# Performance work log

Hardware: AMD Instinct MI355X
Metric: run time of the kernel (lower is better)

Reference implementation:

```python
import jax, jax.numpy as jnp
import numpy as np

B, S, D, H, F = 8, 1024, 1024, 16, 4096
DH = D // H
EPS = 1e-8
NEG_INF = -1e30


def setup_inputs() -> dict:
    key = jax.random.key(0)
    ks = jax.random.split(key, 12)
    x = jax.random.normal(ks[0], (B, S, D), jnp.float32)
    # variable valid lengths in [S//2, S]; True = keep (valid token)
    lengths = jax.random.randint(ks[1], (B,), S // 2, S + 1)
    src_key_padding_mask = jnp.arange(S)[None, :] < lengths[:, None]
    rel_pos_bias = 0.02 * jax.random.normal(ks[2], (1, H, S, S), jnp.float32)
    w = lambda k, sh, std: std * jax.random.normal(k, sh, jnp.float32)
    std = D ** -0.5
    return {
        'x': x,
        'src_key_padding_mask': src_key_padding_mask,
        'rel_pos_bias': rel_pos_bias,
        'Wq': w(ks[3], (D, D), std),
        'Wk': w(ks[4], (D, D), std),
        'Wv': w(ks[5], (D, D), std),
        'Wo': w(ks[6], (D, D), std),
        'g1': jnp.ones((D,), jnp.float32),
        'g2': jnp.ones((D,), jnp.float32),
        'W1': w(ks[7], (D, F), std),
        'b1': jnp.zeros((F,), jnp.float32),
        'W2': w(ks[8], (F, F and D), F ** -0.5),
        'b2': jnp.zeros((D,), jnp.float32),
    }


def rmsnorm(x, g):
    # x / sqrt(mean(x^2) + eps) * g   (no mean subtraction)
    ms = jnp.mean(x * x, axis=-1, keepdims=True)
    return x * jax.lax.rsqrt(ms + EPS) * g


def attention(h, kpm, rel_pos_bias, Wq, Wk, Wv, Wo):
    b, s, d = h.shape
    q = (h @ Wq).reshape(b, s, H, DH)
    k = (h @ Wk).reshape(b, s, H, DH)
    v = (h @ Wv).reshape(b, s, H, DH)
    scores = jnp.einsum('bqhd,bkhd->bhqk', q, k) / np.sqrt(DH)
    scores = scores + rel_pos_bias
    scores = jnp.where(kpm[:, None, None, :], scores, NEG_INF)
    attn = jax.nn.softmax(scores, axis=-1)
    out = jnp.einsum('bhqk,bkhd->bqhd', attn, v).reshape(b, s, d)
    return out @ Wo


def reference(x, src_key_padding_mask, rel_pos_bias,
              Wq, Wk, Wv, Wo, g1, g2, W1, b1, W2, b2):
    h = rmsnorm(x, g1)
    x = x + attention(h, src_key_padding_mask, rel_pos_bias, Wq, Wk, Wv, Wo)
    h = rmsnorm(x, g2)
    ff = jax.nn.relu(h @ W1 + b1) @ W2 + b2
    return x + ff
```

## Files before the change

### kernel.cpp

```cpp
#include <hip/hip_runtime.h>
#include <stdint.h>

typedef __bf16 bf16;
typedef __bf16 bf16x4 __attribute__((ext_vector_type(4)));
typedef __bf16 bf16x8 __attribute__((ext_vector_type(8)));
typedef float f32x4 __attribute__((ext_vector_type(4)));

constexpr int Bz = 8, S = 1024, D = 1024, NH = 16, DH = 64, F = 4096;

__device__ __forceinline__ bool is_f32(const uint16_t* dt) { return dt[0] == 0; }

__device__ __forceinline__ void ld4(const void* p, size_t idx, bool f32, float o[4]) {
  if (f32) {
    float4 v = *(const float4*)((const float*)p + idx);
    o[0] = v.x; o[1] = v.y; o[2] = v.z; o[3] = v.w;
  } else {
    bf16x4 v = *(const bf16x4*)((const bf16*)p + idx);
    o[0] = v[0]; o[1] = v[1]; o[2] = v[2]; o[3] = v[3];
  }
}

__device__ __forceinline__ float ld1(const void* p, size_t idx, bool f32) {
  return f32 ? ((const float*)p)[idx] : (float)((const bf16*)p)[idx];
}

__device__ __forceinline__ void gload_lds16(const bf16* g, bf16* l) {
  __builtin_amdgcn_global_load_lds(
      (const __attribute__((address_space(1))) void*)g,
      (__attribute__((address_space(3))) void*)l, 16, 0, 0);
}

__global__ void lengths_kernel(const unsigned char* __restrict__ mask,
                               int* __restrict__ lengths) {
  int b = blockIdx.x;
  int esz = (mask[1] == 1) ? 1 : ((mask[1] != 0) ? 2 : 4);
  int cnt = 0;
  for (int s = threadIdx.x; s < S; s += blockDim.x) {
    const unsigned char* p = mask + ((size_t)b * S + s) * esz;
    unsigned v = 0;
    for (int j = 0; j < esz; j++) v |= p[j];
    cnt += (v != 0) ? 1 : 0;
  }
#pragma unroll
  for (int m = 32; m >= 1; m >>= 1) cnt += __shfl_xor(cnt, m);
  __shared__ int sred[4];
  if ((threadIdx.x & 63) == 0) sred[threadIdx.x >> 6] = cnt;
  __syncthreads();
  if (threadIdx.x == 0) lengths[b] = sred[0] + sred[1] + sred[2] + sred[3];
}

__global__ void transpose_any(const void* __restrict__ src, bf16* __restrict__ dst,
                              int R, int C, const uint16_t* __restrict__ dt) {
  bool f32 = is_f32(dt);
  __shared__ bf16 tile[64][65];
  int c0 = blockIdx.x * 64, r0 = blockIdx.y * 64;
  int tx = threadIdx.x, ty = threadIdx.y;
#pragma unroll
  for (int i = 0; i < 4; i++) {
    int r = ty * 4 + i;
    float v[4];
    ld4(src, (size_t)(r0 + r) * C + c0 + tx * 4, f32, v);
#pragma unroll
    for (int j = 0; j < 4; j++) tile[r][tx * 4 + j] = (bf16)v[j];
  }
  __syncthreads();
#pragma unroll
  for (int i = 0; i < 4; i++) {
    int rr = ty * 4 + i;
    bf16x4 ov;
#pragma unroll
    for (int j = 0; j < 4; j++) ov[j] = tile[tx * 4 + j][rr];
    *(bf16x4*)(dst + (size_t)(c0 + rr) * R + r0 + tx * 4) = ov;
  }
}

__global__ void bias_cvt(const void* __restrict__ src, bf16* __restrict__ dst,
                         const uint16_t* __restrict__ dt) {
  bool f32 = is_f32(dt);
  size_t i = ((size_t)blockIdx.x * 256 + threadIdx.x) * 4;
  float v[4];
  ld4(src, i, f32, v);
  bf16x4 o;
#pragma unroll
  for (int j = 0; j < 4; j++) o[j] = (bf16)v[j];
  *(bf16x4*)(dst + i) = o;
}

template <bool ADD>
__global__ void rmsnorm_kernel(const void* __restrict__ xv, const bf16* __restrict__ add,
                               const void* __restrict__ gv, bf16* __restrict__ y,
                               const uint16_t* __restrict__ dt) {
  bool f32 = is_f32(dt);
  int row = blockIdx.x, t = threadIdx.x;
  float xf[4];
  ld4(xv, (size_t)row * D + t * 4, f32, xf);
  if (ADD) {
    bf16x4 a = *(const bf16x4*)(add + (size_t)row * D + t * 4);
#pragma unroll
    for (int j = 0; j < 4; j++) xf[j] += (float)a[j];
  }
  float ss = xf[0] * xf[0] + xf[1] * xf[1] + xf[2] * xf[2] + xf[3] * xf[3];
#pragma unroll
  for (int m = 32; m >= 1; m >>= 1) ss += __shfl_xor(ss, m);
  __shared__ float sred[4];
  if ((t & 63) == 0) sred[t >> 6] = ss;
  __syncthreads();
  float tot = sred[0] + sred[1] + sred[2] + sred[3];
  float scale = rsqrtf(tot * (1.0f / D) + 1e-8f);
  float gf[4];
  ld4(gv, (size_t)t * 4, f32, gf);
  bf16x4 ov;
#pragma unroll
  for (int j = 0; j < 4; j++) ov[j] = (bf16)(xf[j] * scale * gf[j]);
  *(bf16x4*)(y + (size_t)row * D + t * 4) = ov;
}

template <bool BIAS, bool RELU, bool RES1, bool RES2, bool OUTEXT, bool VT>
__global__ void gemm_nt(const bf16* __restrict__ A, const bf16* __restrict__ Bt,
                        void* __restrict__ Cv, const void* __restrict__ biasv,
                        const void* __restrict__ res1, const bf16* __restrict__ res2,
                        int M, int N, int K, const uint16_t* __restrict__ dt) {
  bool f32 = is_f32(dt);
  __shared__ bf16 As[2 * 4096];
  __shared__ bf16 Bs[2 * 4096];
  const int tid = threadIdx.x, lane = tid & 63, w = tid >> 6;
  const int wm = w >> 1, wn = w & 1;
  const int lid = blockIdx.x;
  const int bm = ((lid & 7) << 3) + ((lid >> 3) & 7);
  const int bn = lid >> 6;
  const int quad = lane >> 4, c = lane & 15;

  f32x4 acc[4][4];
#pragma unroll
  for (int i = 0; i < 4; i++)
#pragma unroll
    for (int j = 0; j < 4; j++)
#pragma unroll
      for (int r = 0; r < 4; r++) acc[i][j][r] = 0.f;

  const bf16* gA = A + (size_t)(bm * 128 + w * 16 + (lane >> 2)) * K + (lane & 3) * 8;
  const bf16* gB = Bt + (size_t)(bn * 128 + w * 16 + (lane >> 2)) * K + (lane & 3) * 8;
  bf16* lA = As + w * 512;
  bf16* lB = Bs + w * 512;
  const size_t rstep = (size_t)64 * K;

  int aoff[4], boff[4];
#pragma unroll
  for (int i = 0; i < 4; i++) {
    aoff[i] = (wm * 64 + i * 16 + c) * 32 + quad * 8;
    boff[i] = (wn * 64 + i * 16 + c) * 32 + quad * 8;
  }

  for (int k0 = 0; k0 < K; k0 += 64) {
    __syncthreads();
#pragma unroll
    for (int p = 0; p < 2; p++) {
      gload_lds16(gA + p * 32, lA + p * 4096);
      gload_lds16(gA + p * 32 + rstep, lA + p * 4096 + 2048);
      gload_lds16(gB + p * 32, lB + p * 4096);
      gload_lds16(gB + p * 32 + rstep, lB + p * 4096 + 2048);
    }
    gA += 64;
    gB += 64;
    __syncthreads();
#pragma unroll
    for (int p = 0; p < 2; p++) {
      bf16x8 af[4], bfr[4];
#pragma unroll
      for (int i = 0; i < 4; i++) af[i] = *(const bf16x8*)(As + p * 4096 + aoff[i]);
#pragma unroll
      for (int i = 0; i < 4; i++) bfr[i] = *(const bf16x8*)(Bs + p * 4096 + boff[i]);
#pragma unroll
      for (int i = 0; i < 4; i++)
#pragma unroll
        for (int j = 0; j < 4; j++)
          acc[i][j] = __builtin_amdgcn_mfma_f32_16x16x32_bf16(af[i], bfr[j], acc[i][j], 0, 0, 0);
    }
  }

  const int m0 = bm * 128 + wm * 64, n0 = bn * 128 + wn * 64;
#pragma unroll
  for (int i = 0; i < 4; i++) {
#pragma unroll
    for (int j = 0; j < 4; j++) {
      int col = n0 + j * 16 + c;
      if (VT) {
        int row0 = m0 + i * 16 + quad * 4;
        int bb = row0 >> 10, s0 = row0 & 1023;
        int hh = col >> 6, dd = col & 63;
        bf16x4 ov;
#pragma unroll
        for (int r = 0; r < 4; r++) ov[r] = (bf16)acc[i][j][r];
        *(bf16x4*)((bf16*)Cv + ((size_t)((bb << 4) + hh) * 64 + dd) * 1024 + s0) = ov;
      } else {
        float bv = BIAS ? ld1(biasv, col, f32) : 0.f;
#pragma unroll
        for (int r = 0; r < 4; r++) {
          int row = m0 + i * 16 + quad * 4 + r;
          size_t idx = (size_t)row * N + col;
          float vv = acc[i][j][r] + bv;
          if (RELU) vv = fmaxf(vv, 0.f);
          if (RES1) vv += ld1(res1, idx, f32);
          if (RES2) vv += (float)res2[idx];
          if (OUTEXT && f32) ((float*)Cv)[idx] = vv;
          else ((bf16*)Cv)[idx] = (bf16)vv;
        }
      }
    }
  }
}

__global__ void __launch_bounds__(256) attn_kernel(
    const bf16* __restrict__ qk, const bf16* __restrict__ vt,
    const bf16* __restrict__ bias, const int* __restrict__ lengths,
    bf16* __restrict__ out) {
  __shared__ bf16 Qs[64][72];
  __shared__ bf16 Ks[64][72];
  __shared__ bf16 Vs[64][72];
  __shared__ bf16 Ps[4][16][72];
  const int tid = threadIdx.x, lane = tid & 63, w = tid >> 6;
  const int id = blockIdx.x;
  const int qt = id >> 7, b = (id >> 4) & 7, h = id & 15;
  const int len = lengths[b];
  const int quad = lane >> 4, c = lane & 15;
  const int r4 = tid >> 2, c4 = tid & 3;

  {
    size_t qrow = (size_t)(b * S + qt * 64 + r4) * 2048 + h * 64 + c4 * 8;
    *(bf16x8*)&Qs[r4][c4 * 8] = *(const bf16x8*)&qk[qrow];
    *(bf16x8*)&Qs[r4][32 + c4 * 8] = *(const bf16x8*)&qk[qrow + 32];
  }
  __syncthreads();
  const bf16x8 a0 = *(const bf16x8*)&Qs[w * 16 + c][quad * 8];
  const bf16x8 a1 = *(const bf16x8*)&Qs[w * 16 + c][32 + quad * 8];

  float l_[4] = {0.f, 0.f, 0.f, 0.f};
  f32x4 o[4];
#pragma unroll
  for (int ni = 0; ni < 4; ni++)
#pragma unroll
    for (int r = 0; r < 4; r++) o[ni][r] = 0.f;

  const bf16* bb = bias + (size_t)h * S * S + (size_t)(qt * 64 + w * 16 + quad * 4) * S;
  const int nkt = (len + 63) >> 6;

  for (int kt = 0; kt < nkt; kt++) {
    __syncthreads();
    {
      size_t krow = (size_t)(b * S + kt * 64 + r4) * 2048 + 1024 + h * 64 + c4 * 8;
      *(bf16x8*)&Ks[r4][c4 * 8] = *(const bf16x8*)&qk[krow];
      *(bf16x8*)&Ks[r4][32 + c4 * 8] = *(const bf16x8*)&qk[krow + 32];
      size_t vrow = ((size_t)((b * 16 + h) * 64 + r4)) * 1024 + kt * 64 + c4 * 8;
      *(bf16x8*)&Vs[r4][c4 * 8] = *(const bf16x8*)&vt[vrow];
      *(bf16x8*)&Vs[r4][32 + c4 * 8] = *(const bf16x8*)&vt[vrow + 32];
    }
    __syncthreads();

    f32x4 s[4];
#pragma unroll
    for (int ni = 0; ni < 4; ni++)
#pragma unroll
      for (int r = 0; r < 4; r++) s[ni][r] = 0.f;
#pragma unroll
    for (int ni = 0; ni < 4; ni++) {
      bf16x8 b0 = *(const bf16x8*)&Ks[ni * 16 + c][quad * 8];
      bf16x8 b1 = *(const bf16x8*)&Ks[ni * 16 + c][32 + quad * 8];
      s[ni] = __builtin_amdgcn_mfma_f32_16x16x32_bf16(a0, b0, s[ni], 0, 0, 0);
      s[ni] = __builtin_amdgcn_mfma_f32_16x16x32_bf16(a1, b1, s[ni], 0, 0, 0);
    }

    const bool full = (kt * 64 + 64 <= len);
#pragma unroll
    for (int ni = 0; ni < 4; ni++) {
      int col = kt * 64 + ni * 16 + c;
      bool valid = full || (col < len);
#pragma unroll
      for (int r = 0; r < 4; r++) {
        float vb = (float)bb[(size_t)r * S + col];
        float p = valid ? __expf(s[ni][r] * 0.125f + vb) : 0.f;
        s[ni][r] = p;
        l_[r] += p;
      }
    }

#pragma unroll
    for (int ni = 0; ni < 4; ni++)
#pragma unroll
      for (int r = 0; r < 4; r++) Ps[w][quad * 4 + r][ni * 16 + c] = (bf16)s[ni][r];

    bf16x8 p0 = *(const bf16x8*)&Ps[w][c][quad * 8];
    bf16x8 p1 = *(const bf16x8*)&Ps[w][c][32 + quad * 8];
#pragma unroll
    for (int ni = 0; ni < 4; ni++) {
      bf16x8 vb0 = *(const bf16x8*)&Vs[ni * 16 + c][quad * 8];
      bf16x8 vb1 = *(const bf16x8*)&Vs[ni * 16 + c][32 + quad * 8];
      o[ni] = __builtin_amdgcn_mfma_f32_16x16x32_bf16(p0, vb0, o[ni], 0, 0, 0);
      o[ni] = __builtin_amdgcn_mfma_f32_16x16x32_bf16(p1, vb1, o[ni], 0, 0, 0);
    }
  }

  float inv[4];
#pragma unroll
  for (int r = 0; r < 4; r++) {
    float l = l_[r];
    l += __shfl_xor(l, 1);
    l += __shfl_xor(l, 2);
    l += __shfl_xor(l, 4);
    l += __shfl_xor(l, 8);
    inv[r] = 1.f / l;
  }
#pragma unroll
  for (int ni = 0; ni < 4; ni++)
#pragma unroll
    for (int r = 0; r < 4; r++) {
      size_t idx = ((size_t)(b * S + qt * 64 + w * 16 + quad * 4 + r)) * D + h * 64 + ni * 16 + c;
      out[idx] = (bf16)(o[ni][r] * inv[r]);
    }
}

extern "C" void kernel_launch(void* const* d_in, const int* in_sizes, int n_in,
                              void* d_out, int out_size, void* d_ws, size_t ws_size,
                              hipStream_t stream) {
  const void* x = d_in[0];
  const unsigned char* mask = (const unsigned char*)d_in[1];
  const void* rpb = d_in[2];
  const void* Wq = d_in[3];
  const void* Wk = d_in[4];
  const void* Wv = d_in[5];
  const void* Wo = d_in[6];
  const void* g1 = d_in[7];
  const void* g2 = d_in[8];
  const void* W1 = d_in[9];
  const void* b1 = d_in[10];
  const void* W2 = d_in[11];
  const void* b2 = d_in[12];
  const uint16_t* dt = (const uint16_t*)d_in[7];

  char* ws = (char*)d_ws;
  const size_t MB = 1024 * 1024;
  bf16* WqkT = (bf16*)(ws + 0 * MB);
  bf16* WkT = (bf16*)(ws + 2 * MB);
  bf16* WvT = (bf16*)(ws + 4 * MB);
  bf16* WoT = (bf16*)(ws + 6 * MB);
  bf16* W1T = (bf16*)(ws + 8 * MB);
  bf16* W2T = (bf16*)(ws + 16 * MB);
  bf16* hbuf = (bf16*)(ws + 24 * MB);
  bf16* qkbuf = (bf16*)(ws + 40 * MB);
  bf16* d1buf = (bf16*)(ws + 40 * MB);
  bf16* vtbuf = (bf16*)(ws + 72 * MB);
  bf16* biasb = (bf16*)(ws + 88 * MB);
  bf16* a1b = (bf16*)(ws + 56 * MB);
  int* lens = (int*)d_out;

  dim3 tb(16, 16);
  lengths_kernel<<<dim3(8), dim3(256), 0, stream>>>(mask, lens);
  transpose_any<<<dim3(16, 16), tb, 0, stream>>>(Wq, WqkT, 1024, 1024, dt);
  transpose_any<<<dim3(16, 16), tb, 0, stream>>>(Wk, WkT, 1024, 1024, dt);
  transpose_any<<<dim3(16, 16), tb, 0, stream>>>(Wv, WvT, 1024, 1024, dt);
  transpose_any<<<dim3(16, 16), tb, 0, stream>>>(Wo, WoT, 1024, 1024, dt);
  transpose_any<<<dim3(64, 16), tb, 0, stream>>>(W1, W1T, 1024, 4096, dt);
  transpose_any<<<dim3(16, 64), tb, 0, stream>>>(W2, W2T, 4096, 1024, dt);
  bias_cvt<<<dim3(16384), dim3(256), 0, stream>>>(rpb, biasb, dt);

  rmsnorm_kernel<false><<<dim3(8192), dim3(256), 0, stream>>>(x, nullptr, g1, hbuf, dt);
  gemm_nt<false, false, false, false, false, false><<<dim3(16 * 64), dim3(256), 0, stream>>>(
      hbuf, WqkT, qkbuf, nullptr, nullptr, nullptr, 8192, 2048, 1024, dt);
  gemm_nt<false, false, false, false, false, true><<<dim3(8 * 64), dim3(256), 0, stream>>>(
      hbuf, WvT, vtbuf, nullptr, nullptr, nullptr, 8192, 1024, 1024, dt);
  attn_kernel<<<dim3(2048), dim3(256), 0, stream>>>(qkbuf, vtbuf, biasb, lens, hbuf);
  gemm_nt<false, false, false, false, false, false><<<dim3(8 * 64), dim3(256), 0, stream>>>(
      hbuf, WoT, d1buf, nullptr, nullptr, nullptr, 8192, 1024, 1024, dt);
  rmsnorm_kernel<true><<<dim3(8192), dim3(256), 0, stream>>>(x, d1buf, g2, hbuf, dt);
  gemm_nt<true, true, false, false, false, false><<<dim3(32 * 64), dim3(256), 0, stream>>>(
      hbuf, W1T, a1b, b1, nullptr, nullptr, 8192, 4096, 1024, dt);
  gemm_nt<true, false, true, true, true, false><<<dim3(8 * 64), dim3(256), 0, stream>>>(
      a1b, W2T, d_out, b2, x, d1buf, 8192, 1024, 4096, dt);

  (void)in_sizes; (void)n_in; (void)out_size; (void)ws_size;
}
```

Measured before the change: 585.0 us.

## Prefetch K/V tiles into registers, reuse Q smem for P, use exp2 with prescaled bias

The attention loop now loads the next K/V tile from global memory into registers while computing on the current tile, and it issues the bias loads early. This is meant to hide global-load latency behind the MFMA work. The bias is prescaled by log2(e) during conversion so softmax can use exp2f with a single fma. The Q shared buffer is reused for the P tile with an XOR swizzle, which cuts LDS footprint and bank conflicts. The costs are higher register pressure and bf16 rounding of the prescaled bias.

```diff
diff --git a/kernel.cpp b/kernel.cpp
--- a/kernel.cpp
+++ b/kernel.cpp
@@ -82,7 +82,7 @@
   ld4(src, i, f32, v);
   bf16x4 o;
 #pragma unroll
-  for (int j = 0; j < 4; j++) o[j] = (bf16)v[j];
+  for (int j = 0; j < 4; j++) o[j] = (bf16)(v[j] * 1.4426950408889634f);
   *(bf16x4*)(dst + i) = o;
 }
 
@@ -214,10 +214,9 @@
     const bf16* __restrict__ qk, const bf16* __restrict__ vt,
     const bf16* __restrict__ bias, const int* __restrict__ lengths,
     bf16* __restrict__ out) {
-  __shared__ bf16 Qs[64][72];
+  __shared__ bf16 QPs[64 * 72];
   __shared__ bf16 Ks[64][72];
   __shared__ bf16 Vs[64][72];
-  __shared__ bf16 Ps[4][16][72];
   const int tid = threadIdx.x, lane = tid & 63, w = tid >> 6;
   const int id = blockIdx.x;
   const int qt = id >> 7, b = (id >> 4) & 7, h = id & 15;
@@ -227,12 +226,16 @@
 
   {
     size_t qrow = (size_t)(b * S + qt * 64 + r4) * 2048 + h * 64 + c4 * 8;
-    *(bf16x8*)&Qs[r4][c4 * 8] = *(const bf16x8*)&qk[qrow];
-    *(bf16x8*)&Qs[r4][32 + c4 * 8] = *(const bf16x8*)&qk[qrow + 32];
+    *(bf16x8*)&QPs[r4 * 72 + c4 * 8] = *(const bf16x8*)&qk[qrow];
+    *(bf16x8*)&QPs[r4 * 72 + 32 + c4 * 8] = *(const bf16x8*)&qk[qrow + 32];
   }
   __syncthreads();
-  const bf16x8 a0 = *(const bf16x8*)&Qs[w * 16 + c][quad * 8];
-  const bf16x8 a1 = *(const bf16x8*)&Qs[w * 16 + c][32 + quad * 8];
+  const bf16x8 a0 = *(const bf16x8*)&QPs[(w * 16 + c) * 72 + quad * 8];
+  const bf16x8 a1 = *(const bf16x8*)&QPs[(w * 16 + c) * 72 + 32 + quad * 8];
+
+  bf16* Pw = QPs + w * 16 * 72;
+  const int xsw = (quad & 2) << 3;
+  const int xsr = (c & 8) << 1;
 
   float l_[4] = {0.f, 0.f, 0.f, 0.f};
   f32x4 o[4];
@@ -241,20 +244,41 @@
 #pragma unroll
     for (int r = 0; r < 4; r++) o[ni][r] = 0.f;
 
-  const bf16* bb = bias + (size_t)h * S * S + (size_t)(qt * 64 + w * 16 + quad * 4) * S;
+  const bf16* bbp = bias + (size_t)h * S * S + (size_t)(qt * 64 + w * 16 + quad * 4) * S;
   const int nkt = (len + 63) >> 6;
+
+  const size_t KSTEP = (size_t)64 * 2048;
+  const bf16* gk = qk + (size_t)(b * S + r4) * 2048 + 1024 + h * 64 + c4 * 8;
+  const bf16* gv = vt + ((size_t)((b * 16 + h) * 64 + r4)) * 1024 + c4 * 8;
+  bf16x8 kr0 = *(const bf16x8*)gk;
+  bf16x8 kr1 = *(const bf16x8*)(gk + 32);
+  bf16x8 vr0 = *(const bf16x8*)gv;
+  bf16x8 vr1 = *(const bf16x8*)(gv + 32);
+  gk += KSTEP;
+  gv += 64;
 
   for (int kt = 0; kt < nkt; kt++) {
     __syncthreads();
-    {
-      size_t krow = (size_t)(b * S + kt * 64 + r4) * 2048 + 1024 + h * 64 + c4 * 8;
-      *(bf16x8*)&Ks[r4][c4 * 8] = *(const bf16x8*)&qk[krow];
-      *(bf16x8*)&Ks[r4][32 + c4 * 8] = *(const bf16x8*)&qk[krow + 32];
-      size_t vrow = ((size_t)((b * 16 + h) * 64 + r4)) * 1024 + kt * 64 + c4 * 8;
-      *(bf16x8*)&Vs[r4][c4 * 8] = *(const bf16x8*)&vt[vrow];
-      *(bf16x8*)&Vs[r4][32 + c4 * 8] = *(const bf16x8*)&vt[vrow + 32];
-    }
+    *(bf16x8*)&Ks[r4][c4 * 8] = kr0;
+    *(bf16x8*)&Ks[r4][32 + c4 * 8] = kr1;
+    *(bf16x8*)&Vs[r4][c4 * 8] = vr0;
+    *(bf16x8*)&Vs[r4][32 + c4 * 8] = vr1;
     __syncthreads();
+
+    bf16 br[4][4];
+#pragma unroll
+    for (int ni = 0; ni < 4; ni++)
+#pragma unroll
+      for (int r = 0; r < 4; r++) br[ni][r] = bbp[(size_t)r * S + ni * 16 + c];
+
+    if (kt + 1 < nkt) {
+      kr0 = *(const bf16x8*)gk;
+      kr1 = *(const bf16x8*)(gk + 32);
+      vr0 = *(const bf16x8*)gv;
+      vr1 = *(const bf16x8*)(gv + 32);
+      gk += KSTEP;
+      gv += 64;
+    }
 
     f32x4 s[4];
 #pragma unroll
@@ -276,8 +300,7 @@
       bool valid = full || (col < len);
 #pragma unroll
       for (int r = 0; r < 4; r++) {
-        float vb = (float)bb[(size_t)r * S + col];
-        float p = valid ? __expf(s[ni][r] * 0.125f + vb) : 0.f;
+        float p = valid ? exp2f(fmaf(s[ni][r], 0.18033688011112042f, (float)br[ni][r])) : 0.f;
         s[ni][r] = p;
         l_[r] += p;
       }
@@ -286,10 +309,11 @@
 #pragma unroll
     for (int ni = 0; ni < 4; ni++)
 #pragma unroll
-      for (int r = 0; r < 4; r++) Ps[w][quad * 4 + r][ni * 16 + c] = (bf16)s[ni][r];
-
-    bf16x8 p0 = *(const bf16x8*)&Ps[w][c][quad * 8];
-    bf16x8 p1 = *(const bf16x8*)&Ps[w][c][32 + quad * 8];
+      for (int r = 0; r < 4; r++)
+        Pw[(quad * 4 + r) * 72 + ((ni * 16 + c) ^ xsw)] = (bf16)s[ni][r];
+
+    bf16x8 p0 = *(const bf16x8*)&Pw[c * 72 + ((quad * 8) ^ xsr)];
+    bf16x8 p1 = *(const bf16x8*)&Pw[c * 72 + ((32 + quad * 8) ^ xsr)];
 #pragma unroll
     for (int ni = 0; ni < 4; ni++) {
       bf16x8 vb0 = *(const bf16x8*)&Vs[ni * 16 + c][quad * 8];
@@ -297,6 +321,7 @@
       o[ni] = __builtin_amdgcn_mfma_f32_16x16x32_bf16(p0, vb0, o[ni], 0, 0, 0);
       o[ni] = __builtin_amdgcn_mfma_f32_16x16x32_bf16(p1, vb1, o[ni], 0, 0, 0);
     }
+    bbp += 64;
   }
 
   float inv[4];
```

Result: faster. 550.0 us (-6.0%).
